# Optimization experiments

Measured on AMD Instinct MI355X. Metric: run time of the kernel, lower is better.

## Reference

```python
import jax, jax.numpy as jnp
import numpy as np

N_NODES = 100000
N_EDGES = 3200000
IN_SIZE = 256
HID_SIZE = 256
OUT_SIZE = 64


def setup_inputs() -> dict:
    key = jax.random.key(0)
    ks = jax.random.split(key, 8)
    X = jax.random.normal(ks[0], (N_NODES, IN_SIZE), dtype=jnp.float32)
    edge_vals = jax.random.uniform(ks[1], (N_EDGES,), dtype=jnp.float32)
    # xavier-uniform-ish init for weights
    lim1 = float(np.sqrt(6.0 / (IN_SIZE + HID_SIZE)))
    W1 = jax.random.uniform(ks[2], (IN_SIZE, HID_SIZE), minval=-lim1, maxval=lim1, dtype=jnp.float32)
    b1 = jnp.zeros((HID_SIZE,), dtype=jnp.float32)
    lim2 = float(np.sqrt(6.0 / (HID_SIZE + OUT_SIZE)))
    W2 = jax.random.uniform(ks[3], (HID_SIZE, OUT_SIZE), minval=-lim2, maxval=lim2, dtype=jnp.float32)
    b2 = jnp.zeros((OUT_SIZE,), dtype=jnp.float32)
    row = jnp.sort(jax.random.randint(ks[4], (N_EDGES,), 0, N_NODES, dtype=jnp.int32))
    col = jax.random.randint(ks[5], (N_EDGES,), 0, N_NODES, dtype=jnp.int32)
    return {"X": X, "edge_vals": edge_vals, "W1": W1, "b1": b1,
            "W2": W2, "b2": b2, "row": row, "col": col}


def reference(X, edge_vals, W1, b1, W2, b2, row, col):
    """2-layer GCN (eval mode, dropout = identity).

    A is a sparse NxN matrix in COO form: A[row[e], col[e]] = edge_vals[e].
    Layer: relu(A @ (X @ W1) + b1); output: A @ (h @ W2) + b2.
    """
    n = X.shape[0]

    def spmm(dense):  # (A @ dense): gather columns, scale, segment-sum over rows
        gathered = edge_vals[:, None] * dense[col]        # [E, F]
        return jax.ops.segment_sum(gathered, row, num_segments=n)

    h = spmm(X @ W1) + b1          # [N, HID]
    h = jax.nn.relu(h)
    out = spmm(h @ W2) + b2        # [N, OUT]
    return out
```

## Files before the change

### kernel.cpp

```cpp
#include <hip/hip_runtime.h>


constexpr int IN_SIZE = 256;
constexpr int HID = 256;
constexpr int OUTF = 64;

typedef __bf16 bf16x8 __attribute__((ext_vector_type(8)));
typedef float f32x4 __attribute__((ext_vector_type(4)));

__device__ __forceinline__ ushort f2b(float f) {
    uint u = __float_as_uint(f);
    uint r = (u + 0x7fffu + ((u >> 16) & 1u)) >> 16;
    return (ushort)r;
}
__device__ __forceinline__ float b2f(ushort h) {
    return __uint_as_float(((uint)h) << 16);
}

__global__ void setup_kernel(const int* __restrict__ row, int* __restrict__ rp,
                             const float* __restrict__ W1, ushort* __restrict__ W1T,
                             const float* __restrict__ W2, ushort* __restrict__ W2T,
                             int n, int E, int rpB) {
    int b = blockIdx.x;
    if (b < rpB) {
        int i = b * 256 + threadIdx.x;
        if (i > n) return;
        int lo = 0, hi = E;
        while (lo < hi) {
            int mid = (lo + hi) >> 1;
            if (row[mid] < i) lo = mid + 1; else hi = mid;
        }
        rp[i] = lo;
    } else if (b < rpB + 256) {
        int nn = b - rpB;
        int k = threadIdx.x;
        W1T[(size_t)nn * 256 + k] = f2b(W1[(size_t)k * 256 + nn]);
    } else {
        int nn = b - rpB - 256;
        int k = threadIdx.x;
        W2T[(size_t)nn * 256 + k] = f2b(W2[(size_t)k * 64 + nn]);
    }
}

__global__ __launch_bounds__(256, 2)
void gemm1_cast_n256(const float* __restrict__ A, const ushort* __restrict__ Bt,
                     ushort* __restrict__ C, float* __restrict__ s1, int M) {
    constexpr int K = 256;
    __shared__ ushort As[128 * 40];
    __shared__ ushort Bs[256 * 40];
    __shared__ float red[2][128];
    const int tid = threadIdx.x;
    const int wave = tid >> 6, lane = tid & 63;
    const int quad = lane >> 4, l = lane & 15;
    const int wr = wave >> 1, wc = wave & 1;
    const int m0 = blockIdx.x * 128;

    const int ar = tid >> 1;
    const int ah = (tid & 1) * 16;
    const size_t aoff = (size_t)min(m0 + ar, M - 1) * K + ah;
    const int bn = tid >> 2;
    const int bkp = (tid & 3) * 8;

    f32x4 acc[4][8] = {};

    for (int k0 = 0; k0 < K; k0 += 32) {
        float4 a0 = *(const float4*)(A + aoff + k0);
        float4 a1 = *(const float4*)(A + aoff + k0 + 4);
        float4 a2 = *(const float4*)(A + aoff + k0 + 8);
        float4 a3 = *(const float4*)(A + aoff + k0 + 12);
        uint4 bv[4];
#pragma unroll
        for (int j = 0; j < 4; ++j)
            bv[j] = *(const uint4*)(Bt + (size_t)(bn + 64 * j) * K + k0 + bkp);
        uint4 pa0, pa1;
        pa0.x = (uint)f2b(a0.x) | ((uint)f2b(a0.y) << 16);
        pa0.y = (uint)f2b(a0.z) | ((uint)f2b(a0.w) << 16);
        pa0.z = (uint)f2b(a1.x) | ((uint)f2b(a1.y) << 16);
        pa0.w = (uint)f2b(a1.z) | ((uint)f2b(a1.w) << 16);
        pa1.x = (uint)f2b(a2.x) | ((uint)f2b(a2.y) << 16);
        pa1.y = (uint)f2b(a2.z) | ((uint)f2b(a2.w) << 16);
        pa1.z = (uint)f2b(a3.x) | ((uint)f2b(a3.y) << 16);
        pa1.w = (uint)f2b(a3.z) | ((uint)f2b(a3.w) << 16);
        __syncthreads();
        *(uint4*)&As[ar * 40 + ah] = pa0;
        *(uint4*)&As[ar * 40 + ah + 8] = pa1;
#pragma unroll
        for (int j = 0; j < 4; ++j)
            *(uint4*)&Bs[(bn + 64 * j) * 40 + bkp] = bv[j];
        __syncthreads();

        bf16x8 af[4], bfr[8];
        const ushort* ab = &As[(wr * 64 + l) * 40 + quad * 8];
#pragma unroll
        for (int mt = 0; mt < 4; ++mt)
            af[mt] = *(const bf16x8*)(ab + mt * 16 * 40);
        const ushort* bb = &Bs[(wc * 128 + l) * 40 + quad * 8];
#pragma unroll
        for (int nt = 0; nt < 8; ++nt)
            bfr[nt] = *(const bf16x8*)(bb + nt * 16 * 40);
#pragma unroll
        for (int mt = 0; mt < 4; ++mt)
#pragma unroll
            for (int nt = 0; nt < 8; ++nt)
                acc[mt][nt] = __builtin_amdgcn_mfma_f32_16x16x32_bf16(
                    af[mt], bfr[nt], acc[mt][nt], 0, 0, 0);
    }

    float rmax[4][4];
#pragma unroll
    for (int mt = 0; mt < 4; ++mt)
#pragma unroll
        for (int reg = 0; reg < 4; ++reg) {
            float m = 0.f;
#pragma unroll
            for (int nt = 0; nt < 8; ++nt)
                m = fmaxf(m, fabsf(acc[mt][nt][reg]));
            rmax[mt][reg] = m;
        }
#pragma unroll
    for (int mt = 0; mt < 4; ++mt)
#pragma unroll
        for (int nt = 0; nt < 8; ++nt)
#pragma unroll
            for (int reg = 0; reg < 4; ++reg) {
                int r = m0 + wr * 64 + mt * 16 + quad * 4 + reg;
                int c = wc * 128 + nt * 16 + l;
                if (r < M) C[(size_t)r * 256 + c] = f2b(acc[mt][nt][reg]);
            }
#pragma unroll
    for (int s = 1; s <= 8; s <<= 1)
#pragma unroll
        for (int mt = 0; mt < 4; ++mt)
#pragma unroll
            for (int reg = 0; reg < 4; ++reg)
                rmax[mt][reg] = fmaxf(rmax[mt][reg], __shfl_xor(rmax[mt][reg], s));
    if (l < 4) {
#pragma unroll
        for (int mt = 0; mt < 4; ++mt)
            red[wc][wr * 64 + mt * 16 + quad * 4 + l] = rmax[mt][l];
    }
    __syncthreads();
    if (tid < 128) {
        int r = m0 + tid;
        if (r < M) s1[r] = fmaxf(red[0][tid], red[1][tid]) * (1.f / 127.f);
    }
}

__global__ __launch_bounds__(256, 4)
void gemm2_bf16(const ushort* __restrict__ A, const ushort* __restrict__ Bt,
                ushort* __restrict__ C, float* __restrict__ s2, int M) {
    constexpr int K = 256;
    __shared__ ushort As[128 * 40];
    __shared__ ushort Bs[64 * 40];
    __shared__ float red[2][128];
    const int tid = threadIdx.x;
    const int wave = tid >> 6, lane = tid & 63;
    const int quad = lane >> 4, l = lane & 15;
    const int wr = wave >> 1, wc = wave & 1;
    const int m0 = blockIdx.x * 128;

    const int crow = tid >> 2;
    const int cpart = (tid & 3) * 8;
    const size_t aoff0 = (size_t)min(m0 + crow, M - 1) * K + cpart;
    const size_t aoff1 = (size_t)min(m0 + crow + 64, M - 1) * K + cpart;
    const size_t boff  = (size_t)crow * K + cpart;

    f32x4 acc[4][2] = {};

    for (int k0 = 0; k0 < K; k0 += 32) {
        uint4 a0 = *(const uint4*)(A + aoff0 + k0);
        uint4 a1 = *(const uint4*)(A + aoff1 + k0);
        uint4 b0 = *(const uint4*)(Bt + boff + k0);
        __syncthreads();
        *(uint4*)&As[crow * 40 + cpart] = a0;
        *(uint4*)&As[(crow + 64) * 40 + cpart] = a1;
        *(uint4*)&Bs[crow * 40 + cpart] = b0;
        __syncthreads();

        bf16x8 af[4], bfr[2];
        const ushort* ab = &As[(wr * 64 + l) * 40 + quad * 8];
#pragma unroll
        for (int mt = 0; mt < 4; ++mt)
            af[mt] = *(const bf16x8*)(ab + mt * 16 * 40);
        const ushort* bb = &Bs[(wc * 32 + l) * 40 + quad * 8];
#pragma unroll
        for (int nt = 0; nt < 2; ++nt)
            bfr[nt] = *(const bf16x8*)(bb + nt * 16 * 40);
#pragma unroll
        for (int mt = 0; mt < 4; ++mt)
#pragma unroll
            for (int nt = 0; nt < 2; ++nt)
                acc[mt][nt] = __builtin_amdgcn_mfma_f32_16x16x32_bf16(
                    af[mt], bfr[nt], acc[mt][nt], 0, 0, 0);
    }

    float rmax[4][4];
#pragma unroll
    for (int mt = 0; mt < 4; ++mt)
#pragma unroll
        for (int reg = 0; reg < 4; ++reg)
            rmax[mt][reg] = fmaxf(fabsf(acc[mt][0][reg]), fabsf(acc[mt][1][reg]));
#pragma unroll
    for (int mt = 0; mt < 4; ++mt)
#pragma unroll
        for (int nt = 0; nt < 2; ++nt)
#pragma unroll
            for (int reg = 0; reg < 4; ++reg) {
                int r = m0 + wr * 64 + mt * 16 + quad * 4 + reg;
                int c = wc * 32 + nt * 16 + l;
                if (r < M) C[(size_t)r * 64 + c] = f2b(acc[mt][nt][reg]);
            }
#pragma unroll
    for (int s = 1; s <= 8; s <<= 1)
#pragma unroll
        for (int mt = 0; mt < 4; ++mt)
#pragma unroll
            for (int reg = 0; reg < 4; ++reg)
                rmax[mt][reg] = fmaxf(rmax[mt][reg], __shfl_xor(rmax[mt][reg], s));
    if (l < 4) {
#pragma unroll
        for (int mt = 0; mt < 4; ++mt)
            red[wc][wr * 64 + mt * 16 + quad * 4 + l] = rmax[mt][l];
    }
    __syncthreads();
    if (tid < 128) {
        int r = m0 + tid;
        if (r < M) s2[r] = fmaxf(red[0][tid], red[1][tid]) * (1.f / 127.f);
    }
}

__global__ __launch_bounds__(256)
void fuse_quant_prep(const ushort* __restrict__ Sb, const float* __restrict__ s,
                     char* __restrict__ Q, int total_elems,
                     const float* __restrict__ vals, const int* __restrict__ col,
                     int2* __restrict__ ew, int E, int quantBlocks, int logw) {
    int b = blockIdx.x;
    if (b < quantBlocks) {
        int i = (b * 256 + threadIdx.x) * 8;
        if (i >= total_elems) return;
        int r = i >> logw;
        float sc = s[r];
        float inv = sc > 0.f ? 1.f / sc : 0.f;
        uint4 x = *(const uint4*)(Sb + i);
        float f[8];
        f[0] = b2f((ushort)x.x); f[1] = b2f((ushort)(x.x >> 16));
        f[2] = b2f((ushort)x.y); f[3] = b2f((ushort)(x.y >> 16));
        f[4] = b2f((ushort)x.z); f[5] = b2f((ushort)(x.z >> 16));
        f[6] = b2f((ushort)x.w); f[7] = b2f((ushort)(x.w >> 16));
        uint2 o;
        o.x = ((uint)((int)rintf(f[0] * inv) & 0xff)) |
              ((uint)((int)rintf(f[1] * inv) & 0xff) << 8) |
              ((uint)((int)rintf(f[2] * inv) & 0xff) << 16) |
              ((uint)((int)rintf(f[3] * inv) & 0xff) << 24);
        o.y = ((uint)((int)rintf(f[4] * inv) & 0xff)) |
              ((uint)((int)rintf(f[5] * inv) & 0xff) << 8) |
              ((uint)((int)rintf(f[6] * inv) & 0xff) << 16) |
              ((uint)((int)rintf(f[7] * inv) & 0xff) << 24);
        *(uint2*)(Q + i) = o;
    } else {
        int e = (b - quantBlocks) * 256 + threadIdx.x;
        if (e >= E) return;
        int c = col[e];
        ew[e] = make_int2(c, __float_as_int(vals[e] * s[c]));
    }
}

__global__ __launch_bounds__(256)
void spmm1_q(const char* __restrict__ Q, const int2* __restrict__ ew,
             const int* __restrict__ rp, const float* __restrict__ bias,
             ushort* __restrict__ H, int n) {
    const int wave = threadIdx.x >> 6;
    const int lane = threadIdx.x & 63;
    const int node = blockIdx.x * 4 + wave;
    if (node >= n) return;
    const int e0 = rp[node], e1 = rp[node + 1];
    float a0 = 0.f, a1 = 0.f, a2 = 0.f, a3 = 0.f;
    int e = e0;
    for (; e + 7 < e1; e += 8) {
#pragma unroll
        for (int u = 0; u < 8; ++u) {
            int2 m = ew[e + u];
            float w = __int_as_float(m.y);
            char4 q = *(const char4*)(Q + (size_t)m.x * 256 + lane * 4);
            a0 += w * (float)q.x;
            a1 += w * (float)q.y;
            a2 += w * (float)q.z;
            a3 += w * (float)q.w;
        }
    }
    for (; e < e1; ++e) {
        int2 m = ew[e];
        float w = __int_as_float(m.y);
        char4 q = *(const char4*)(Q + (size_t)m.x * 256 + lane * 4);
        a0 += w * (float)q.x;
        a1 += w * (float)q.y;
        a2 += w * (float)q.z;
        a3 += w * (float)q.w;
    }
    float4 b = *(const float4*)(bias + lane * 4);
    ushort4 r;
    r.x = f2b(fmaxf(a0 + b.x, 0.f));
    r.y = f2b(fmaxf(a1 + b.y, 0.f));
    r.z = f2b(fmaxf(a2 + b.z, 0.f));
    r.w = f2b(fmaxf(a3 + b.w, 0.f));
    *(ushort4*)(H + (size_t)node * 256 + lane * 4) = r;
}

__global__ __launch_bounds__(256)
void spmm2_q(const char* __restrict__ Q, const int2* __restrict__ ew,
             const int* __restrict__ rp, const float* __restrict__ bias,
             float* __restrict__ O, int n) {
    const int wave = threadIdx.x >> 6;
    const int lane = threadIdx.x & 63;
    const int node = blockIdx.x * 4 + wave;
    if (node >= n) return;
    const int e0 = rp[node], e1 = rp[node + 1];
    float acc = 0.f;
    int e = e0;
    for (; e + 15 < e1; e += 16) {
#pragma unroll
        for (int u = 0; u < 16; ++u) {
            int2 m = ew[e + u];
            acc += __int_as_float(m.y) * (float)Q[(size_t)m.x * 64 + lane];
        }
    }
    for (; e + 3 < e1; e += 4) {
#pragma unroll
        for (int u = 0; u < 4; ++u) {
            int2 m = ew[e + u];
            acc += __int_as_float(m.y) * (float)Q[(size_t)m.x * 64 + lane];
        }
    }
    for (; e < e1; ++e) {
        int2 m = ew[e];
        acc += __int_as_float(m.y) * (float)Q[(size_t)m.x * 64 + lane];
    }
    O[(size_t)node * 64 + lane] = acc + bias[lane];
}

static inline size_t alignup(size_t x) { return (x + 255) & ~(size_t)255; }

extern "C" void kernel_launch(void* const* d_in, const int* in_sizes, int n_in,
                              void* d_out, int out_size, void* d_ws, size_t ws_size,
                              hipStream_t stream) {
    const float* X  = (const float*)d_in[0];
    const float* ev = (const float*)d_in[1];
    const float* W1 = (const float*)d_in[2];
    const float* b1 = (const float*)d_in[3];
    const float* W2 = (const float*)d_in[4];
    const float* b2 = (const float*)d_in[5];
    const int*  row = (const int*)d_in[6];
    const int*  col = (const int*)d_in[7];
    float* out = (float*)d_out;

    const int n = in_sizes[0] / IN_SIZE;
    const int E = in_sizes[1];

    char* p = (char*)d_ws;
    ushort* bufA = (ushort*)p; p += alignup((size_t)n * HID * 2);
    char*   Q1   = (char*)p;   p += alignup((size_t)n * HID);
    float*  s1   = (float*)p;  p += alignup((size_t)n * 4);
    ushort* hw2  = (ushort*)p; p += alignup((size_t)n * OUTF * 2);
    char*   Q2   = (char*)p;   p += alignup((size_t)n * OUTF);
    float*  s2   = (float*)p;  p += alignup((size_t)n * 4);
    ushort* W1T  = (ushort*)p; p += alignup((size_t)IN_SIZE * HID * 2);
    ushort* W2T  = (ushort*)p; p += alignup((size_t)HID * OUTF * 2);
    int*    rp   = (int*)p;    p += alignup((size_t)(n + 1) * 4);
    int2*   ewb  = (int2*)p;   p += alignup((size_t)E * 8);

    const int rpB = (n + 1 + 255) / 256;
    setup_kernel<<<rpB + 256 + 64, 256, 0, stream>>>(row, rp, W1, W1T, W2, W2T,
                                                     n, E, rpB);

    gemm1_cast_n256<<<(n + 127) / 128, 256, 0, stream>>>(X, W1T, bufA, s1, n);

    {
        int qB = ((n * HID / 8) + 255) / 256;
        int pB = (E + 255) / 256;
        fuse_quant_prep<<<qB + pB, 256, 0, stream>>>(bufA, s1, Q1, n * HID,
                                                     ev, col, ewb, E, qB, 8);
    }

    spmm1_q<<<(n + 3) / 4, 256, 0, stream>>>(Q1, ewb, rp, b1, bufA, n);

    gemm2_bf16<<<(n + 127) / 128, 256, 0, stream>>>(bufA, W2T, hw2, s2, n);

    {
        int qB = ((n * OUTF / 8) + 255) / 256;
        int pB = (E + 255) / 256;
        fuse_quant_prep<<<qB + pB, 256, 0, stream>>>(hw2, s2, Q2, n * OUTF,
                                                     ev, col, ewb, E, qB, 6);
    }

    spmm2_q<<<(n + 3) / 4, 256, 0, stream>>>(Q2, ewb, rp, b2, out, n);
}
```

Baseline: 509.5 us.

## Fuse int8 quantization into GEMM epilogues and drop bf16 intermediates

```diff
diff --git a/kernel.cpp b/kernel.cpp
--- a/kernel.cpp
+++ b/kernel.cpp
@@ -42,66 +42,64 @@
     }
 }
 
-__global__ __launch_bounds__(256, 2)
-void gemm1_cast_n256(const float* __restrict__ A, const ushort* __restrict__ Bt,
-                     ushort* __restrict__ C, float* __restrict__ s1, int M) {
+__global__ void prep_edges(const float* __restrict__ vals, const int* __restrict__ col,
+                           const float* __restrict__ s, int2* __restrict__ ew,
+                           int E, int shift) {
+    int e = blockIdx.x * 256 + threadIdx.x;
+    if (e >= E) return;
+    int c = col[e];
+    ew[e] = make_int2(c << shift, __float_as_int(vals[e] * s[c]));
+}
+
+__global__ __launch_bounds__(512)
+void gemm1_q(const float* __restrict__ A, const ushort* __restrict__ Bt,
+             char* __restrict__ Q, float* __restrict__ s1, int M) {
     constexpr int K = 256;
     __shared__ ushort As[128 * 40];
     __shared__ ushort Bs[256 * 40];
-    __shared__ float red[2][128];
+    __shared__ float red[4][128];
+    __shared__ float fin[128];
     const int tid = threadIdx.x;
     const int wave = tid >> 6, lane = tid & 63;
     const int quad = lane >> 4, l = lane & 15;
-    const int wr = wave >> 1, wc = wave & 1;
+    const int wr = wave >> 2, wc = wave & 3;
     const int m0 = blockIdx.x * 128;
 
-    const int ar = tid >> 1;
-    const int ah = (tid & 1) * 16;
-    const size_t aoff = (size_t)min(m0 + ar, M - 1) * K + ah;
+    const int ar = tid >> 2;
+    const int ak = (tid & 3) * 8;
+    const size_t aoff = (size_t)min(m0 + ar, M - 1) * K + ak;
     const int bn = tid >> 2;
     const int bkp = (tid & 3) * 8;
 
-    f32x4 acc[4][8] = {};
+    f32x4 acc[4][4] = {};
 
     for (int k0 = 0; k0 < K; k0 += 32) {
         float4 a0 = *(const float4*)(A + aoff + k0);
         float4 a1 = *(const float4*)(A + aoff + k0 + 4);
-        float4 a2 = *(const float4*)(A + aoff + k0 + 8);
-        float4 a3 = *(const float4*)(A + aoff + k0 + 12);
-        uint4 bv[4];
-#pragma unroll
-        for (int j = 0; j < 4; ++j)
-            bv[j] = *(const uint4*)(Bt + (size_t)(bn + 64 * j) * K + k0 + bkp);
-        uint4 pa0, pa1;
-        pa0.x = (uint)f2b(a0.x) | ((uint)f2b(a0.y) << 16);
-        pa0.y = (uint)f2b(a0.z) | ((uint)f2b(a0.w) << 16);
-        pa0.z = (uint)f2b(a1.x) | ((uint)f2b(a1.y) << 16);
-        pa0.w = (uint)f2b(a1.z) | ((uint)f2b(a1.w) << 16);
-        pa1.x = (uint)f2b(a2.x) | ((uint)f2b(a2.y) << 16);
-        pa1.y = (uint)f2b(a2.z) | ((uint)f2b(a2.w) << 16);
-        pa1.z = (uint)f2b(a3.x) | ((uint)f2b(a3.y) << 16);
-        pa1.w = (uint)f2b(a3.z) | ((uint)f2b(a3.w) << 16);
+        uint4 bv0 = *(const uint4*)(Bt + (size_t)bn * K + k0 + bkp);
+        uint4 bv1 = *(const uint4*)(Bt + (size_t)(bn + 128) * K + k0 + bkp);
+        uint4 pa;
+        pa.x = (uint)f2b(a0.x) | ((uint)f2b(a0.y) << 16);
+        pa.y = (uint)f2b(a0.z) | ((uint)f2b(a0.w) << 16);
+        pa.z = (uint)f2b(a1.x) | ((uint)f2b(a1.y) << 16);
+        pa.w = (uint)f2b(a1.z) | ((uint)f2b(a1.w) << 16);
         __syncthreads();
-        *(uint4*)&As[ar * 40 + ah] = pa0;
-        *(uint4*)&As[ar * 40 + ah + 8] = pa1;
-#pragma unroll
-        for (int j = 0; j < 4; ++j)
-            *(uint4*)&Bs[(bn + 64 * j) * 40 + bkp] = bv[j];
+        *(uint4*)&As[ar * 40 + ak] = pa;
+        *(uint4*)&Bs[bn * 40 + bkp] = bv0;
+        *(uint4*)&Bs[(bn + 128) * 40 + bkp] = bv1;
         __syncthreads();
 
-        bf16x8 af[4], bfr[8];
-        const ushort* ab = &As[(wr * 64 + l) * 40 + quad * 8];
-#pragma unroll
-        for (int mt = 0; mt < 4; ++mt)
-            af[mt] = *(const bf16x8*)(ab + mt * 16 * 40);
-        const ushort* bb = &Bs[(wc * 128 + l) * 40 + quad * 8];
-#pragma unroll
-        for (int nt = 0; nt < 8; ++nt)
-            bfr[nt] = *(const bf16x8*)(bb + nt * 16 * 40);
-#pragma unroll
-        for (int mt = 0; mt < 4; ++mt)
-#pragma unroll
-            for (int nt = 0; nt < 8; ++nt)
+        bf16x8 af[4], bfr[4];
+#pragma unroll
+        for (int mt = 0; mt < 4; ++mt)
+            af[mt] = *(const bf16x8*)&As[(wr * 64 + mt * 16 + l) * 40 + quad * 8];
+#pragma unroll
+        for (int nt = 0; nt < 4; ++nt)
+            bfr[nt] = *(const bf16x8*)&Bs[(wc * 64 + nt * 16 + l) * 40 + quad * 8];
+#pragma unroll
+        for (int mt = 0; mt < 4; ++mt)
+#pragma unroll
+            for (int nt = 0; nt < 4; ++nt)
                 acc[mt][nt] = __builtin_amdgcn_mfma_f32_16x16x32_bf16(
                     af[mt], bfr[nt], acc[mt][nt], 0, 0, 0);
     }
@@ -113,20 +111,10 @@
         for (int reg = 0; reg < 4; ++reg) {
             float m = 0.f;
 #pragma unroll
-            for (int nt = 0; nt < 8; ++nt)
+            for (int nt = 0; nt < 4; ++nt)
                 m = fmaxf(m, fabsf(acc[mt][nt][reg]));
             rmax[mt][reg] = m;
         }
-#pragma unroll
-    for (int mt = 0; mt < 4; ++mt)
-#pragma unroll
-        for (int nt = 0; nt < 8; ++nt)
-#pragma unroll
-            for (int reg = 0; reg < 4; ++reg) {
-                int r = m0 + wr * 64 + mt * 16 + quad * 4 + reg;
-                int c = wc * 128 + nt * 16 + l;
-                if (r < M) C[(size_t)r * 256 + c] = f2b(acc[mt][nt][reg]);
-            }
 #pragma unroll
     for (int s = 1; s <= 8; s <<= 1)
 #pragma unroll
@@ -141,18 +129,39 @@
     }
     __syncthreads();
     if (tid < 128) {
+        float m = fmaxf(fmaxf(red[0][tid], red[1][tid]),
+                        fmaxf(red[2][tid], red[3][tid]));
+        fin[tid] = m;
         int r = m0 + tid;
-        if (r < M) s1[r] = fmaxf(red[0][tid], red[1][tid]) * (1.f / 127.f);
-    }
+        if (r < M) s1[r] = m * (1.f / 127.f);
+    }
+    __syncthreads();
+
+#pragma unroll
+    for (int mt = 0; mt < 4; ++mt)
+#pragma unroll
+        for (int reg = 0; reg < 4; ++reg) {
+            int rl = wr * 64 + mt * 16 + quad * 4 + reg;
+            int r = m0 + rl;
+            if (r >= M) continue;
+            float m = fin[rl];
+            float inv = m > 0.f ? 127.f / m : 0.f;
+#pragma unroll
+            for (int nt = 0; nt < 4; ++nt) {
+                int c = wc * 64 + nt * 16 + l;
+                Q[(size_t)r * 256 + c] = (char)(int)rintf(acc[mt][nt][reg] * inv);
+            }
+        }
 }
 
 __global__ __launch_bounds__(256, 4)
-void gemm2_bf16(const ushort* __restrict__ A, const ushort* __restrict__ Bt,
-                ushort* __restrict__ C, float* __restrict__ s2, int M) {
+void gemm2_q(const ushort* __restrict__ A, const ushort* __restrict__ Bt,
+             char* __restrict__ Q, float* __restrict__ s2, int M) {
     constexpr int K = 256;
     __shared__ ushort As[128 * 40];
     __shared__ ushort Bs[64 * 40];
     __shared__ float red[2][128];
+    __shared__ float fin[128];
     const int tid = threadIdx.x;
     const int wave = tid >> 6, lane = tid & 63;
     const int quad = lane >> 4, l = lane & 15;
@@ -201,16 +210,6 @@
         for (int reg = 0; reg < 4; ++reg)
             rmax[mt][reg] = fmaxf(fabsf(acc[mt][0][reg]), fabsf(acc[mt][1][reg]));
 #pragma unroll
-    for (int mt = 0; mt < 4; ++mt)
-#pragma unroll
-        for (int nt = 0; nt < 2; ++nt)
-#pragma unroll
-            for (int reg = 0; reg < 4; ++reg) {
-                int r = m0 + wr * 64 + mt * 16 + quad * 4 + reg;
-                int c = wc * 32 + nt * 16 + l;
-                if (r < M) C[(size_t)r * 64 + c] = f2b(acc[mt][nt][reg]);
-            }
-#pragma unroll
     for (int s = 1; s <= 8; s <<= 1)
 #pragma unroll
         for (int mt = 0; mt < 4; ++mt)
@@ -224,45 +223,28 @@
     }
     __syncthreads();
     if (tid < 128) {
+        float m = fmaxf(red[0][tid], red[1][tid]);
+        fin[tid] = m;
         int r = m0 + tid;
-        if (r < M) s2[r] = fmaxf(red[0][tid], red[1][tid]) * (1.f / 127.f);
-    }
-}
-
-__global__ __launch_bounds__(256)
-void fuse_quant_prep(const ushort* __restrict__ Sb, const float* __restrict__ s,
-                     char* __restrict__ Q, int total_elems,
-                     const float* __restrict__ vals, const int* __restrict__ col,
-                     int2* __restrict__ ew, int E, int quantBlocks, int logw) {
-    int b = blockIdx.x;
-    if (b < quantBlocks) {
-        int i = (b * 256 + threadIdx.x) * 8;
-        if (i >= total_elems) return;
-        int r = i >> logw;
-        float sc = s[r];
-        float inv = sc > 0.f ? 1.f / sc : 0.f;
-        uint4 x = *(const uint4*)(Sb + i);
-        float f[8];
-        f[0] = b2f((ushort)x.x); f[1] = b2f((ushort)(x.x >> 16));
-        f[2] = b2f((ushort)x.y); f[3] = b2f((ushort)(x.y >> 16));
-        f[4] = b2f((ushort)x.z); f[5] = b2f((ushort)(x.z >> 16));
-        f[6] = b2f((ushort)x.w); f[7] = b2f((ushort)(x.w >> 16));
-        uint2 o;
-        o.x = ((uint)((int)rintf(f[0] * inv) & 0xff)) |
-              ((uint)((int)rintf(f[1] * inv) & 0xff) << 8) |
-              ((uint)((int)rintf(f[2] * inv) & 0xff) << 16) |
-              ((uint)((int)rintf(f[3] * inv) & 0xff) << 24);
-        o.y = ((uint)((int)rintf(f[4] * inv) & 0xff)) |
-              ((uint)((int)rintf(f[5] * inv) & 0xff) << 8) |
-              ((uint)((int)rintf(f[6] * inv) & 0xff) << 16) |
-              ((uint)((int)rintf(f[7] * inv) & 0xff) << 24);
-        *(uint2*)(Q + i) = o;
-    } else {
-        int e = (b - quantBlocks) * 256 + threadIdx.x;
-        if (e >= E) return;
-        int c = col[e];
-        ew[e] = make_int2(c, __float_as_int(vals[e] * s[c]));
-    }
+        if (r < M) s2[r] = m * (1.f / 127.f);
+    }
+    __syncthreads();
+
+#pragma unroll
+    for (int mt = 0; mt < 4; ++mt)
+#pragma unroll
+        for (int reg = 0; reg < 4; ++reg) {
+            int rl = wr * 64 + mt * 16 + quad * 4 + reg;
+            int r = m0 + rl;
+            if (r >= M) continue;
+            float m = fin[rl];
+            float inv = m > 0.f ? 127.f / m : 0.f;
+#pragma unroll
+            for (int nt = 0; nt < 2; ++nt) {
+                int c = wc * 32 + nt * 16 + l;
+                Q[(size_t)r * 64 + c] = (char)(int)rintf(acc[mt][nt][reg] * inv);
+            }
+        }
 }
 
 __global__ __launch_bounds__(256)
@@ -281,7 +263,7 @@
         for (int u = 0; u < 8; ++u) {
             int2 m = ew[e + u];
             float w = __int_as_float(m.y);
-            char4 q = *(const char4*)(Q + (size_t)m.x * 256 + lane * 4);
+            char4 q = *(const char4*)(Q + (size_t)(uint)m.x + lane * 4);
             a0 += w * (float)q.x;
             a1 += w * (float)q.y;
             a2 += w * (float)q.z;
@@ -291,7 +273,7 @@
     for (; e < e1; ++e) {
         int2 m = ew[e];
         float w = __int_as_float(m.y);
-        char4 q = *(const char4*)(Q + (size_t)m.x * 256 + lane * 4);
+        char4 q = *(const char4*)(Q + (size_t)(uint)m.x + lane * 4);
         a0 += w * (float)q.x;
         a1 += w * (float)q.y;
         a2 += w * (float)q.z;
@@ -321,19 +303,19 @@
 #pragma unroll
         for (int u = 0; u < 16; ++u) {
             int2 m = ew[e + u];
-            acc += __int_as_float(m.y) * (float)Q[(size_t)m.x * 64 + lane];
+            acc += __int_as_float(m.y) * (float)Q[(size_t)(uint)m.x + lane];
         }
     }
     for (; e + 3 < e1; e += 4) {
 #pragma unroll
         for (int u = 0; u < 4; ++u) {
             int2 m = ew[e + u];
-            acc += __int_as_float(m.y) * (float)Q[(size_t)m.x * 64 + lane];
+            acc += __int_as_float(m.y) * (float)Q[(size_t)(uint)m.x + lane];
         }
     }
     for (; e < e1; ++e) {
         int2 m = ew[e];
-        acc += __int_as_float(m.y) * (float)Q[(size_t)m.x * 64 + lane];
+        acc += __int_as_float(m.y) * (float)Q[(size_t)(uint)m.x + lane];
     }
     O[(size_t)node * 64 + lane] = acc + bias[lane];
 }
@@ -357,10 +339,9 @@
     const int E = in_sizes[1];
 
     char* p = (char*)d_ws;
-    ushort* bufA = (ushort*)p; p += alignup((size_t)n * HID * 2);
+    ushort* H    = (ushort*)p; p += alignup((size_t)n * HID * 2);
     char*   Q1   = (char*)p;   p += alignup((size_t)n * HID);
     float*  s1   = (float*)p;  p += alignup((size_t)n * 4);
-    ushort* hw2  = (ushort*)p; p += alignup((size_t)n * OUTF * 2);
     char*   Q2   = (char*)p;   p += alignup((size_t)n * OUTF);
     float*  s2   = (float*)p;  p += alignup((size_t)n * 4);
     ushort* W1T  = (ushort*)p; p += alignup((size_t)IN_SIZE * HID * 2);
@@ -372,25 +353,15 @@
     setup_kernel<<<rpB + 256 + 64, 256, 0, stream>>>(row, rp, W1, W1T, W2, W2T,
                                                      n, E, rpB);
 
-    gemm1_cast_n256<<<(n + 127) / 128, 256, 0, stream>>>(X, W1T, bufA, s1, n);
-
-    {
-        int qB = ((n * HID / 8) + 255) / 256;
-        int pB = (E + 255) / 256;
-        fuse_quant_prep<<<qB + pB, 256, 0, stream>>>(bufA, s1, Q1, n * HID,
-                                                     ev, col, ewb, E, qB, 8);
-    }
-
-    spmm1_q<<<(n + 3) / 4, 256, 0, stream>>>(Q1, ewb, rp, b1, bufA, n);
-
-    gemm2_bf16<<<(n + 127) / 128, 256, 0, stream>>>(bufA, W2T, hw2, s2, n);
-
-    {
-        int qB = ((n * OUTF / 8) + 255) / 256;
-        int pB = (E + 255) / 256;
-        fuse_quant_prep<<<qB + pB, 256, 0, stream>>>(hw2, s2, Q2, n * OUTF,
-                                                     ev, col, ewb, E, qB, 6);
-    }
+    gemm1_q<<<(n + 127) / 128, 512, 0, stream>>>(X, W1T, Q1, s1, n);
+
+    prep_edges<<<(E + 255) / 256, 256, 0, stream>>>(ev, col, s1, ewb, E, 8);
+
+    spmm1_q<<<(n + 3) / 4, 256, 0, stream>>>(Q1, ewb, rp, b1, H, n);
+
+    gemm2_q<<<(n + 127) / 128, 256, 0, stream>>>(H, W2T, Q2, s2, n);
+
+    prep_edges<<<(E + 255) / 256, 256, 0, stream>>>(ev, col, s2, ewb, E, 6);
 
     spmm2_q<<<(n + 3) / 4, 256, 0, stream>>>(Q2, ewb, rp, b2, out, n);
 }
```

New measurement: 470.9 us. -7.6%, faster.
